# Kernel optimization log

Hardware: AMD Instinct MI355X
Metric: run time of the kernel (lower is better)

## Reference

```python
import jax, jax.numpy as jnp
import numpy as np
from itertools import combinations

# Static conv hyperparameters (match init_kwargs)
KH = KW = 3
SH = SW = 1
PH = PW = 1
DH = DW = 1
MAJ_DIM = 3  # = kernel_size[0]


def _maj_sim(x):
    """Vectorized bipolar majority-gate simulation. x: [B, n] -> [B].
    result = sum over majority subsets of prod((1+x)_in, (1-x)_out) / 2^(n-1) - 1
    """
    n = x.shape[1]
    thresh = (n + 1) // 2
    one_plus = 1.0 + x
    one_minus = 1.0 - x
    res = jnp.zeros(x.shape[0], dtype=x.dtype)
    for k in range(thresh, n + 1):
        for combo in combinations(range(n), k):
            mask = np.zeros(n, dtype=bool)
            mask[list(combo)] = True
            res = res + jnp.prod(jnp.where(jnp.asarray(mask), one_plus, one_minus), axis=1)
    return res / (2.0 ** (n - 1)) - 1.0


def _stack_maj_sim(x, maj_dim):
    """Stacked majority tree reduction along dim 1. x: [B, n] -> [B, n_final]."""
    B = x.shape[0]
    while x.shape[1] >= maj_dim:
        num_chunks = x.shape[1] // maj_dim
        if num_chunks == 0:
            break
        z = x[:, : num_chunks * maj_dim].reshape(B * num_chunks, maj_dim)
        x = _maj_sim(z).reshape(B, num_chunks)
    return x


def _unfold(x):
    """torch.nn.functional.unfold equivalent. x:[N,C,H,W] -> [N, C*KH*KW, L].
    Feature ordering matches torch: c-major, then kernel row, then kernel col."""
    N, C, H, W = x.shape
    H_out = (H + 2 * PH - DH * (KH - 1) - 1) // SH + 1
    W_out = (W + 2 * PW - DW * (KW - 1) - 1) // SW + 1
    xp = jnp.pad(x, ((0, 0), (0, 0), (PH, PH), (PW, PW)))
    slabs = [
        xp[:, :, i * DH : i * DH + SH * (H_out - 1) + 1 : SH,
              j * DW : j * DW + SW * (W_out - 1) + 1 : SW]
        for i in range(KH) for j in range(KW)
    ]
    p = jnp.stack(slabs, axis=2)  # [N, C, KH*KW, H_out, W_out]
    return p.reshape(N, C * KH * KW, H_out * W_out)


def setup_inputs() -> dict:
    key = jax.random.key(0)
    k1, k2 = jax.random.split(key)
    x = jax.random.normal(k1, (2, 27, 64, 64), dtype=jnp.float32)
    # kaiming-uniform-ish scale for fan_in = 27*3*3 = 243
    weight = jax.random.normal(k2, (32, 27, 3, 3), dtype=jnp.float32) * 0.06
    return {"x": x, "weight": weight}


def reference(x, weight):
    N, C, H, W = x.shape
    OC = weight.shape[0]
    H_out = (H + 2 * PH - DH * (KH - 1) - 1) // SH + 1
    W_out = (W + 2 * PW - DW * (KW - 1) - 1) // SW + 1
    patches = _unfold(x)                       # [N, F, L], F = C*KH*KW
    weight_flat = weight.reshape(OC, -1)       # [OC, F]
    # prod: [N, OC, F, L]
    prod = patches[:, None, :, :] * weight_flat[None, :, :, None]
    F_ = prod.shape[2]
    L = prod.shape[3]
    # reduce the feature dim via stacked majority simulation
    z = prod.transpose(0, 1, 3, 2).reshape(N * OC * L, F_)
    out = _stack_maj_sim(z, MAJ_DIM)           # [N*OC*L, 1]
    return out.reshape(N, OC, H_out, W_out)
```

## Files before the change

kernel.cpp:

```cpp
#include <hip/hip_runtime.h>

#define CIN 27
#define HH 64
#define WW 64
#define OC 32
#define TW 16
#define TH 16
#define RS 20
#define CS (18 * RS)
#define WS 12

__device__ __forceinline__ float maj3(float a, float b, float c) {
    float s = a + b + c;
    return 0.5f * fmaf(-(a * b), c, s);
}

__device__ __forceinline__ float2 pk_maj3(float2 a, float2 b, float2 c) {
    float2 r;
    r.x = maj3(a.x, b.x, c.x);
    r.y = maj3(a.y, b.y, c.y);
    return r;
}

__global__ __launch_bounds__(128) void sconv_maj_kernel(
    const float* __restrict__ x,
    const float* __restrict__ wgt,
    float* __restrict__ out)
{
    __shared__ __align__(16) float sw[CIN * WS];
    __shared__ __align__(16) float sx[CIN * CS];

    const int tx = threadIdx.x;
    const int ty = threadIdx.y;
    const int tid = ty * 8 + tx;
    const int tile_w0 = blockIdx.x * TW;
    const int tile_h0 = blockIdx.y * TH;
    const int n  = blockIdx.z >> 5;
    const int oc = blockIdx.z & 31;

    for (int i = tid; i < CIN * 9; i += 128) {
        int c = i / 9;
        int k = i - 9 * c;
        sw[c * WS + k] = wgt[oc * (CIN * 9) + i];
    }

    const float* xn = x + (size_t)n * (CIN * HH * WW);
    for (int pos = tid; pos < 18 * 18; pos += 128) {
        int r   = pos / 18;
        int col = pos - 18 * r;
        int gr = tile_h0 + r - 1;
        int gc = tile_w0 + col - 1;
        bool ok = ((unsigned)gr < (unsigned)HH) & ((unsigned)gc < (unsigned)WW);
        int off = ok ? (gr * WW + gc) : 0;
        float* lp = sx + r * RS + col;
        #pragma unroll
        for (int c = 0; c < CIN; ++c) {
            float raw = xn[(size_t)c * (HH * WW) + off];
            lp[c * CS] = ok ? raw : 0.0f;
        }
    }
    __syncthreads();

    float2 m4[3];
    #pragma unroll
    for (int q = 0; q < 3; ++q) {
        float2 m3[3];
        #pragma unroll
        for (int t = 0; t < 3; ++t) {
            float2 m2[3];
            #pragma unroll
            for (int u = 0; u < 3; ++u) {
                const int c = q * 9 + t * 3 + u;
                float4 wa = *(const float4*)&sw[c * WS];
                float4 wb = *(const float4*)&sw[c * WS + 4];
                float  w8 = sw[c * WS + 8];
                const float wk[9] = {wa.x, wa.y, wa.z, wa.w,
                                     wb.x, wb.y, wb.z, wb.w, w8};
                float2 m1[3];
                #pragma unroll
                for (int ki = 0; ki < 3; ++ki) {
                    const float2* prow =
                        (const float2*)&sx[c * CS + (ty + ki) * RS + 2 * tx];
                    float2 v01 = prow[0];
                    float2 v23 = prow[1];
                    float w0 = wk[ki * 3 + 0];
                    float w1 = wk[ki * 3 + 1];
                    float w2 = wk[ki * 3 + 2];
                    float2 p0 = make_float2(v01.x * w0, v01.y * w0);
                    float2 p1 = make_float2(v01.y * w1, v23.x * w1);
                    float2 p2 = make_float2(v23.x * w2, v23.y * w2);
                    m1[ki] = pk_maj3(p0, p1, p2);
                }
                m2[u] = pk_maj3(m1[0], m1[1], m1[2]);
            }
            m3[t] = pk_maj3(m2[0], m2[1], m2[2]);
        }
        m4[q] = pk_maj3(m3[0], m3[1], m3[2]);
    }
    float2 res = pk_maj3(m4[0], m4[1], m4[2]);

    const int h = tile_h0 + ty;
    const int w = tile_w0 + 2 * tx;
    float2* po = (float2*)(out + (((size_t)n * OC + oc) * HH + h) * WW + w);
    *po = res;
}

extern "C" void kernel_launch(void* const* d_in, const int* in_sizes, int n_in,
                              void* d_out, int out_size, void* d_ws, size_t ws_size,
                              hipStream_t stream) {
    const float* x   = (const float*)d_in[0];
    const float* wgt = (const float*)d_in[1];
    float* out = (float*)d_out;

    dim3 block(8, 16, 1);
    dim3 grid(WW / TW, HH / TH, 2 * OC);
    sconv_maj_kernel<<<grid, block, 0, stream>>>(x, wgt, out);
}
```

Baseline: 69.94 us.

## Split channel groups across blocks and combine partial majorities in second kernel

Splits the 27-channel majority tree into three 9-channel groups, each computed by a separate block, which triples the grid and cuts shared memory per block so more blocks fit per CU. Each group writes its partial majority result to workspace, and a second elementwise kernel applies the final maj3 across the three partials. This adds a second launch and a round trip of three output-sized buffers through global memory in exchange for more parallelism and occupancy.

```diff
diff --git a/kernel.cpp b/kernel.cpp
--- a/kernel.cpp
+++ b/kernel.cpp
@@ -1,6 +1,7 @@
 #include <hip/hip_runtime.h>
 
 #define CIN 27
+#define CG  9
 #define HH 64
 #define WW 64
 #define OC 32
@@ -9,6 +10,7 @@
 #define RS 20
 #define CS (18 * RS)
 #define WS 12
+#define NPIX (2 * OC * HH * WW)
 
 __device__ __forceinline__ float maj3(float a, float b, float c) {
     float s = a + b + c;
@@ -22,26 +24,29 @@
     return r;
 }
 
-__global__ __launch_bounds__(128) void sconv_maj_kernel(
+__global__ __launch_bounds__(128, 6) void sconv_part_kernel(
     const float* __restrict__ x,
     const float* __restrict__ wgt,
-    float* __restrict__ out)
+    float* __restrict__ part)
 {
-    __shared__ __align__(16) float sw[CIN * WS];
-    __shared__ __align__(16) float sx[CIN * CS];
+    __shared__ __align__(16) float sw[CG * WS];
+    __shared__ __align__(16) float sx[CG * CS];
 
     const int tx = threadIdx.x;
     const int ty = threadIdx.y;
     const int tid = ty * 8 + tx;
     const int tile_w0 = blockIdx.x * TW;
     const int tile_h0 = blockIdx.y * TH;
-    const int n  = blockIdx.z >> 5;
-    const int oc = blockIdx.z & 31;
+    const int noc = blockIdx.z & 63;
+    const int q   = blockIdx.z >> 6;
+    const int n  = noc >> 5;
+    const int oc = noc & 31;
+    const int cbase = q * CG;
 
-    for (int i = tid; i < CIN * 9; i += 128) {
-        int c = i / 9;
-        int k = i - 9 * c;
-        sw[c * WS + k] = wgt[oc * (CIN * 9) + i];
+    if (tid < CG * 9) {
+        int c = tid / 9;
+        int k = tid - 9 * c;
+        sw[c * WS + k] = wgt[oc * (CIN * 9) + (cbase + c) * 9 + k];
     }
 
     const float* xn = x + (size_t)n * (CIN * HH * WW);
@@ -54,55 +59,67 @@
         int off = ok ? (gr * WW + gc) : 0;
         float* lp = sx + r * RS + col;
         #pragma unroll
-        for (int c = 0; c < CIN; ++c) {
-            float raw = xn[(size_t)c * (HH * WW) + off];
+        for (int c = 0; c < CG; ++c) {
+            float raw = xn[(size_t)(cbase + c) * (HH * WW) + off];
             lp[c * CS] = ok ? raw : 0.0f;
         }
     }
     __syncthreads();
 
-    float2 m4[3];
+    float2 m3[3];
     #pragma unroll
-    for (int q = 0; q < 3; ++q) {
-        float2 m3[3];
+    for (int t = 0; t < 3; ++t) {
+        float2 m2[3];
         #pragma unroll
-        for (int t = 0; t < 3; ++t) {
-            float2 m2[3];
+        for (int u = 0; u < 3; ++u) {
+            const int c = t * 3 + u;
+            float4 wa = *(const float4*)&sw[c * WS];
+            float4 wb = *(const float4*)&sw[c * WS + 4];
+            float  w8 = sw[c * WS + 8];
+            const float wk[9] = {wa.x, wa.y, wa.z, wa.w,
+                                 wb.x, wb.y, wb.z, wb.w, w8};
+            float2 m1[3];
             #pragma unroll
-            for (int u = 0; u < 3; ++u) {
-                const int c = q * 9 + t * 3 + u;
-                float4 wa = *(const float4*)&sw[c * WS];
-                float4 wb = *(const float4*)&sw[c * WS + 4];
-                float  w8 = sw[c * WS + 8];
-                const float wk[9] = {wa.x, wa.y, wa.z, wa.w,
-                                     wb.x, wb.y, wb.z, wb.w, w8};
-                float2 m1[3];
-                #pragma unroll
-                for (int ki = 0; ki < 3; ++ki) {
-                    const float2* prow =
-                        (const float2*)&sx[c * CS + (ty + ki) * RS + 2 * tx];
-                    float2 v01 = prow[0];
-                    float2 v23 = prow[1];
-                    float w0 = wk[ki * 3 + 0];
-                    float w1 = wk[ki * 3 + 1];
-                    float w2 = wk[ki * 3 + 2];
-                    float2 p0 = make_float2(v01.x * w0, v01.y * w0);
-                    float2 p1 = make_float2(v01.y * w1, v23.x * w1);
-                    float2 p2 = make_float2(v23.x * w2, v23.y * w2);
-                    m1[ki] = pk_maj3(p0, p1, p2);
-                }
-                m2[u] = pk_maj3(m1[0], m1[1], m1[2]);
+            for (int ki = 0; ki < 3; ++ki) {
+                const float2* prow =
+                    (const float2*)&sx[c * CS + (ty + ki) * RS + 2 * tx];
+                float2 v01 = prow[0];
+                float2 v23 = prow[1];
+                float w0 = wk[ki * 3 + 0];
+                float w1 = wk[ki * 3 + 1];
+                float w2 = wk[ki * 3 + 2];
+                float2 p0 = make_float2(v01.x * w0, v01.y * w0);
+                float2 p1 = make_float2(v01.y * w1, v23.x * w1);
+                float2 p2 = make_float2(v23.x * w2, v23.y * w2);
+                m1[ki] = pk_maj3(p0, p1, p2);
             }
-            m3[t] = pk_maj3(m2[0], m2[1], m2[2]);
+            m2[u] = pk_maj3(m1[0], m1[1], m1[2]);
         }
-        m4[q] = pk_maj3(m3[0], m3[1], m3[2]);
+        m3[t] = pk_maj3(m2[0], m2[1], m2[2]);
     }
-    float2 res = pk_maj3(m4[0], m4[1], m4[2]);
+    float2 m4 = pk_maj3(m3[0], m3[1], m3[2]);
 
     const int h = tile_h0 + ty;
     const int w = tile_w0 + 2 * tx;
-    float2* po = (float2*)(out + (((size_t)n * OC + oc) * HH + h) * WW + w);
-    *po = res;
+    float2* po = (float2*)(part + (size_t)q * NPIX + ((size_t)noc * HH + h) * WW + w);
+    *po = m4;
+}
+
+__global__ __launch_bounds__(256) void sconv_combine_kernel(
+    const float* __restrict__ part,
+    float* __restrict__ out)
+{
+    const int i = blockIdx.x * 256 + threadIdx.x;
+    const float4* p0 = (const float4*)part;
+    const float4* p1 = (const float4*)(part + NPIX);
+    const float4* p2 = (const float4*)(part + 2 * (size_t)NPIX);
+    float4 a = p0[i], b = p1[i], c = p2[i];
+    float4 r;
+    r.x = maj3(a.x, b.x, c.x);
+    r.y = maj3(a.y, b.y, c.y);
+    r.z = maj3(a.z, b.z, c.z);
+    r.w = maj3(a.w, b.w, c.w);
+    ((float4*)out)[i] = r;
 }
 
 extern "C" void kernel_launch(void* const* d_in, const int* in_sizes, int n_in,
@@ -110,9 +127,12 @@
                               hipStream_t stream) {
     const float* x   = (const float*)d_in[0];
     const float* wgt = (const float*)d_in[1];
-    float* out = (float*)d_out;
+    float* out  = (float*)d_out;
+    float* part = (float*)d_ws;
 
     dim3 block(8, 16, 1);
-    dim3 grid(WW / TW, HH / TH, 2 * OC);
-    sconv_maj_kernel<<<grid, block, 0, stream>>>(x, wgt, out);
+    dim3 grid(WW / TW, HH / TH, 3 * 2 * OC);
+    sconv_part_kernel<<<grid, block, 0, stream>>>(x, wgt, part);
+
+    sconv_combine_kernel<<<NPIX / 4 / 256, 256, 0, stream>>>(part, out);
 }
```

After: 70.56 us. Within noise of the previous version (+0.9%).
